# Kernel optimization log

Hardware: AMD Instinct MI355X
Metric: run time of the kernel (lower is better)

The kernel has to match this reference:

```python
import jax, jax.numpy as jnp
import numpy as np

B, L, DIN = 2048, 70, 15
HID, NF, K = 16, 4, 40          # hidden_units//2, n_features, kernel_size
C = DIN + 1 + NF                # 20 signature input channels (original + time + conv features)
Z0 = 64
SIG_CH = C + C * C + C ** 3     # 8420, depth-3 signature channels


def setup_inputs() -> dict:
    key = jax.random.key(0)
    ks = jax.random.split(key, 8)
    return {
        "observed_data": jax.random.normal(ks[0], (B, L, DIN), jnp.float32),
        "observed_tp": jnp.linspace(0.0, 1.0, L, dtype=jnp.float32),
        "conv1_w": jax.random.normal(ks[1], (HID, DIN, K), jnp.float32) / np.float32(np.sqrt(DIN * K)),
        "conv1_b": jnp.zeros((HID,), jnp.float32),
        "conv2_w": jax.random.normal(ks[2], (HID, HID), jnp.float32) / np.float32(np.sqrt(HID)),
        "conv2_b": jnp.zeros((HID,), jnp.float32),
        "conv3_w": jax.random.normal(ks[3], (NF, HID), jnp.float32) / np.float32(np.sqrt(HID)),
        "conv3_b": jnp.zeros((NF,), jnp.float32),
        "w_out": jax.random.normal(ks[4], (2 * Z0, SIG_CH), jnp.float32) * np.float32(np.sqrt(2.0 / (SIG_CH + 2 * Z0))),
        "b_out": jnp.zeros((2 * Z0,), jnp.float32),
    }


def _augment(x, w1, b1, w2, b2, w3, b3):
    # x: (B, L, DIN).  signatory.Augment: conv(K) -> relu -> conv1x1 -> relu -> conv1x1,
    # then concat [truncated original, time channel, conv features] along channels.
    xc = jnp.transpose(x, (0, 2, 1))                                   # (B, DIN, L)
    h = jax.lax.conv_general_dilated(xc, w1, (1,), 'VALID')            # (B, HID, Lp)
    h = h + b1[None, :, None]
    h = jnp.einsum('oc,bcl->bol', w2, jax.nn.relu(h)) + b2[None, :, None]
    h = jnp.einsum('oc,bcl->bol', w3, jax.nn.relu(h)) + b3[None, :, None]
    conv_out = jnp.transpose(h, (0, 2, 1))                             # (B, Lp, NF)
    Lp = conv_out.shape[1]
    orig = x[:, K - 1:, :]                                             # (B, Lp, DIN)
    t = jnp.linspace(0.0, 1.0, Lp, dtype=x.dtype)
    time = jnp.broadcast_to(t[None, :, None], (x.shape[0], Lp, 1))
    return jnp.concatenate([orig, time, conv_out], axis=2)             # (B, Lp, C)


def _signature_depth3(path):
    # Truncated (depth 3) path signature with basepoint=True, via Chen's identity:
    # S <- S \otimes exp(dx) over increments, zero basepoint prepended.
    incs = jnp.diff(path, axis=1, prepend=jnp.zeros_like(path[:, :1]))  # (B, Lp, C)
    incs = jnp.transpose(incs, (1, 0, 2))                               # (Lp, B, C)
    Bn, Cn = path.shape[0], path.shape[2]
    s1 = jnp.zeros((Bn, Cn), path.dtype)
    s2 = jnp.zeros((Bn, Cn, Cn), path.dtype)
    s3 = jnp.zeros((Bn, Cn, Cn, Cn), path.dtype)

    def step(carry, d):
        s1, s2, s3 = carry
        e2 = 0.5 * d[:, :, None] * d[:, None, :]                        # d\otimes d / 2
        e3 = (e2[:, :, :, None] * d[:, None, None, :]) / 3.0            # d^{\otimes 3} / 6
        n3 = (s3
              + s2[:, :, :, None] * d[:, None, None, :]
              + s1[:, :, None, None] * e2[:, None, :, :]
              + e3)
        n2 = s2 + s1[:, :, None] * d[:, None, :] + e2
        n1 = s1 + d
        return (n1, n2, n3), None

    (s1, s2, s3), _ = jax.lax.scan(step, (s1, s2, s3), incs)
    return jnp.concatenate([s1, s2.reshape(Bn, -1), s3.reshape(Bn, -1)], axis=1)


def reference(observed_data, observed_tp, conv1_w, conv1_b, conv2_w, conv2_b,
              conv3_w, conv3_b, w_out, b_out):
    # encode_obs_time=False -> observed_tp unused
    path = _augment(observed_data, conv1_w, conv1_b, conv2_w, conv2_b, conv3_w, conv3_b)
    sig = _signature_depth3(path)                                       # (B, SIG_CH)
    z = sig @ w_out.T + b_out                                           # (B, 2*Z0)
    mean_z0 = z[:, :Z0][None]                                           # (1, B, Z0)
    std_z0 = jax.nn.softplus(z[:, Z0:][None])                           # (1, B, Z0)
    return mean_z0, std_z0
```

## Files before the change

kernel.cpp:

```cpp
#include <hip/hip_runtime.h>
#include <math.h>

#define B_TOT 2048
#define D_INC 15
#define KW    40
#define CCH   20
#define LP    31
#define SIGCH 8420
#define SIGP  8448
#define NOUT  128
#define KSPLIT 11
#define KLEN  768

typedef _Float16 f16;
typedef _Float16 f16x8 __attribute__((ext_vector_type(8)));
typedef _Float16 f16x4 __attribute__((ext_vector_type(4)));
typedef _Float16 f16x2 __attribute__((ext_vector_type(2)));
typedef float    f32x4 __attribute__((ext_vector_type(4)));

__global__ __launch_bounds__(256) void k_prep(const float* __restrict__ w1,
                                              const float* __restrict__ w_out,
                                              f16* __restrict__ wA,
                                              f16* __restrict__ wh)
{
    if (blockIdx.x == 0) {
        const int ln = threadIdx.x & 63;
        const int wv = threadIdx.x >> 6;
        const int h  = ln & 15;
        const int q4 = ln >> 4;
        for (int gi = 0; gi < 5; ++gi) {
            int g = wv * 5 + gi;
            f16x8 v;
#pragma unroll
            for (int j = 0; j < 8; ++j) {
                int kq = q4 * 8 + j;
                int kk = 2 * g + (kq >> 4);
                int c  = kq & 15;
                v[j] = (c < D_INC) ? (f16)w1[h * 600 + c * 40 + kk] : (f16)0.f;
            }
            *(f16x8*)(wA + g * 512 + ln * 8) = v;
        }
        return;
    }
    int t0 = (blockIdx.x - 1) * 256 + threadIdx.x;
    for (int chunk = t0; chunk < 128 * 1056; chunk += 8192) {
        int o  = chunk / 1056;
        int cw = chunk - o * 1056;
        int c0 = cw * 8;
        f16x8 v;
        if (c0 + 8 <= SIGCH) {
            const float* src = w_out + (size_t)o * SIGCH + c0;
            float4 a = *(const float4*)src;
            float4 b = *(const float4*)(src + 4);
            v = (f16x8){(f16)a.x,(f16)a.y,(f16)a.z,(f16)a.w,
                        (f16)b.x,(f16)b.y,(f16)b.z,(f16)b.w};
        } else {
#pragma unroll
            for (int e = 0; e < 8; ++e) {
                int c = c0 + e;
                v[e] = (c < SIGCH) ? (f16)w_out[(size_t)o * SIGCH + c] : (f16)0.f;
            }
        }
        *(f16x8*)(wh + (size_t)o * SIGP + c0) = v;
    }
}

__global__ __launch_bounds__(256, 3) void k_augsig(
    const float* __restrict__ x,  const f16* __restrict__ wA, const float* __restrict__ b1,
    const float* __restrict__ w2, const float* __restrict__ b2,
    const float* __restrict__ w3, const float* __restrict__ b3,
    f16* __restrict__ sig)
{
    __shared__ float pool[12388];
    float* xs    = pool;
    f16*   xp16  = (f16*)(pool + 4272);
    float* h1s   = (float*)xp16;
    float* pprev = pool + 9408;
    float* wsmall= pool + 12032;
    float* w2s = wsmall;        float* b2s = wsmall + 256;
    float* w3s = wsmall + 272;  float* b3s = wsmall + 336;
    float* b1s = wsmall + 340;

    const int tid  = threadIdx.x;
    const int b0   = blockIdx.x * 4;
    const int lane = tid & 63;
    const int w    = tid >> 6;
    const int n16  = lane & 15;
    const int q4   = lane >> 4;

    for (int i = tid; i < 4 * 1050; i += 256) {
        int bl = i / 1050; int t = i - bl * 1050;
        xs[bl * 1068 + t] = x[(size_t)b0 * 1050 + i];
    }
    if (tid < 256) w2s[tid] = w2[tid];
    if (tid < 16)  b2s[tid] = b2[tid];
    if (tid < 64)  w3s[tid] = w3[tid];
    if (tid < 4)   b3s[tid] = b3[tid];
    if (tid < 16)  b1s[tid] = b1[tid];

    f16x8 wa[20];
#pragma unroll
    for (int g = 0; g < 20; ++g) wa[g] = *(const f16x8*)(wA + g * 512 + lane * 8);
    __syncthreads();

    for (int r = tid; r < 280; r += 256) {
        int bl = r / 70; int pos = r - bl * 70;
        const float* src = xs + bl * 1068 + pos * 15;
        f16* dst = xp16 + bl * 1152 + pos * 16;
#pragma unroll
        for (int c = 0; c < 15; ++c) dst[c] = (f16)src[c];
        dst[15] = (f16)0.f;
    }
    __syncthreads();

    f32x4 cacc[2];
#pragma unroll
    for (int tile = 0; tile < 2; ++tile) {
        const int pos0 = tile * 15;
        f32x4 acc = {0.f, 0.f, 0.f, 0.f};
#pragma unroll
        for (int g = 0; g < 20; ++g) {
            const f16x8 bf = *(const f16x8*)&xp16[w * 1152 +
                (pos0 + n16 + 2 * g + (q4 >> 1)) * 16 + (q4 & 1) * 8];
            acc = __builtin_amdgcn_mfma_f32_16x16x32_f16(wa[g], bf, acc, 0, 0, 0);
        }
        cacc[tile] = acc;
    }
    __syncthreads();

#pragma unroll
    for (int tile = 0; tile < 2; ++tile) {
        int pos = tile * 15 + n16;
#pragma unroll
        for (int r = 0; r < 4; ++r) {
            int h = q4 * 4 + r;
            h1s[(w * 31 + pos) * 17 + h] = fmaxf(cacc[tile][r] + b1s[h], 0.f);
        }
    }
    __syncthreads();

    if (tid < 124) {
        const int bl2 = tid / 31;
        const int pos = tid - bl2 * 31;
        float hr[16];
#pragma unroll
        for (int c2 = 0; c2 < 16; ++c2) hr[c2] = h1s[tid * 17 + c2];
        float h2[16];
#pragma unroll
        for (int o = 0; o < 16; ++o) {
            float s = b2s[o];
#pragma unroll
            for (int c2 = 0; c2 < 16; ++c2) s += w2s[o * 16 + c2] * hr[c2];
            h2[o] = fmaxf(s, 0.f);
        }
        float h3[4];
#pragma unroll
        for (int f = 0; f < 4; ++f) {
            float s = b3s[f];
#pragma unroll
            for (int c2 = 0; c2 < 16; ++c2) s += w3s[f * 16 + c2] * h2[c2];
            h3[f] = s;
        }
        float* pr = pprev + bl2 * 656 + 20 + pos * 20;
#pragma unroll
        for (int d = 0; d < D_INC; ++d) pr[d] = xs[bl2 * 1068 + (pos + 39) * 15 + d];
        pr[15] = (float)pos * (1.0f / 30.0f);
#pragma unroll
        for (int f = 0; f < 4; ++f) pr[16 + f] = h3[f];
    } else {
        int z = tid - 124;
        if (z < 80) pprev[(z / 20) * 656 + (z % 20)] = 0.f;
    }
    __syncthreads();

    float* pp   = pprev + w * 656;
    f16*   scr  = (f16*)pool + w * 4704;
    f16*   dtr  = scr;
    f16*   atr  = scr + 800;
    f16*   etr  = scr + 1600;
    f16*   Vb   = scr + 2400;

    for (int e = lane; e < 620; e += 64) {
        int c = e / 31, t = e - c * 31;
        float p0 = pp[t * 20 + c];
        float d  = pp[(t + 1) * 20 + c] - p0;
        dtr[c * 40 + t] = (f16)d;
        atr[c * 40 + t] = (f16)(p0 + 0.5f * d);
        etr[c * 40 + t] = (f16)(0.5f * p0 + d * (1.0f / 6.0f));
    }
    if (lane < 20) {
        dtr[lane * 40 + 31] = (f16)0.f;
        atr[lane * 40 + 31] = (f16)0.f;
        etr[lane * 40 + 31] = (f16)0.f;
    }
    __syncthreads();

    if (lane < 20) {
        f16* vr = Vb + lane * 72;
        float s = 0.f;
        for (int t = 30; t >= 0; --t) {
            float dv = (float)dtr[lane * 40 + t];
            vr[t]      = (f16)s;
            vr[32 + t] = (f16)dv;
            s += dv;
        }
        vr[31] = (f16)0.f;
        vr[63] = (f16)0.f;
    } else if (lane == 20) {
        f16* vr = Vb + 20 * 72;
        for (int k = 0; k < 64; ++k) vr[k] = (k < 31) ? (f16)1.f : (f16)0.f;
    }
    for (int e = lane; e < 11 * 32; e += 64) {
        int row = 21 + (e >> 5);
        int kk  = (e & 31) * 2;
        *(f16x2*)(Vb + row * 72 + kk) = (f16x2){(f16)0.f, (f16)0.f};
    }
    __syncthreads();

    f16x8 bf[2][2];
#pragma unroll
    for (int kc = 0; kc < 2; ++kc)
#pragma unroll
        for (int nt = 0; nt < 2; ++nt)
            bf[kc][nt] = *(const f16x8*)(Vb + (nt * 16 + n16) * 72 + kc * 32 + q4 * 8);

    const int b = b0 + w;
    f16* sg = sig + (size_t)b * SIGP;

    for (int mt = 0; mt < 25; ++mt) {
        const int p = mt * 16 + n16;
        const int i = p / 20, j = p - i * 20;
        f16x8 av = *(const f16x8*)(atr + i * 40 + q4 * 8);
        f16x8 ev = *(const f16x8*)(etr + i * 40 + q4 * 8);
        f16x8 dv = *(const f16x8*)(dtr + j * 40 + q4 * 8);
        f16x8 uf = av * dv;
        f16x8 ef = ev * dv;

        f32x4 a0 = {0.f,0.f,0.f,0.f}, a1 = {0.f,0.f,0.f,0.f};
        a0 = __builtin_amdgcn_mfma_f32_16x16x32_f16(bf[0][0], uf, a0, 0, 0, 0);
        a0 = __builtin_amdgcn_mfma_f32_16x16x32_f16(bf[1][0], ef, a0, 0, 0, 0);
        a1 = __builtin_amdgcn_mfma_f32_16x16x32_f16(bf[0][1], uf, a1, 0, 0, 0);
        a1 = __builtin_amdgcn_mfma_f32_16x16x32_f16(bf[1][1], ef, a1, 0, 0, 0);

        f16x4 s0 = {(f16)a0[0], (f16)a0[1], (f16)a0[2], (f16)a0[3]};
        *(f16x4*)(sg + 420 + p * 20 + q4 * 4) = s0;
        if (q4 == 0) {
            f16x4 s1v = {(f16)a1[0], (f16)a1[1], (f16)a1[2], (f16)a1[3]};
            *(f16x4*)(sg + 420 + p * 20 + 16) = s1v;
        } else if (q4 == 1) {
            sg[20 + p] = (f16)a1[0];
        }
    }

    if (lane < 20) sg[lane] = (f16)pp[620 + lane];
    if (lane < 28) sg[SIGCH + lane] = (f16)0.f;
}

__global__ __launch_bounds__(256, 4) void k_gemm(const f16* __restrict__ sigh,
                                                 const f16* __restrict__ wh,
                                                 float* __restrict__ z_part)
{
    const int tid = threadIdx.x;
    const int l   = tid & 63;
    const int wv  = tid >> 6;
    const int mt  = blockIdx.x / KSPLIT;
    const int s   = blockIdx.x - mt * KSPLIT;
    const int m0  = mt * 32;
    const int kb  = s * KLEN;
    const int kg   = l >> 4;
    const int mrow = l & 15;

    const f16* a0p = sigh + (size_t)(m0 + mrow) * SIGP + kb + kg * 8;
    const f16* a1p = a0p + (size_t)16 * SIGP;
    const f16* b0p = wh   + (size_t)(wv * 32 + mrow) * SIGP + kb + kg * 8;
    const f16* b1p = b0p + (size_t)16 * SIGP;

    const f32x4 z4 = {0.f, 0.f, 0.f, 0.f};
    f32x4 acc[2][2];
    acc[0][0] = z4; acc[0][1] = z4; acc[1][0] = z4; acc[1][1] = z4;

#pragma unroll 2
    for (int ks = 0; ks < 24; ++ks) {
        const int ko = ks * 32;
        f16x8 aF0 = *(const f16x8*)(a0p + ko);
        f16x8 aF1 = *(const f16x8*)(a1p + ko);
        f16x8 bF0 = *(const f16x8*)(b0p + ko);
        f16x8 bF1 = *(const f16x8*)(b1p + ko);
        acc[0][0] = __builtin_amdgcn_mfma_f32_16x16x32_f16(aF0, bF0, acc[0][0], 0, 0, 0);
        acc[0][1] = __builtin_amdgcn_mfma_f32_16x16x32_f16(aF0, bF1, acc[0][1], 0, 0, 0);
        acc[1][0] = __builtin_amdgcn_mfma_f32_16x16x32_f16(aF1, bF0, acc[1][0], 0, 0, 0);
        acc[1][1] = __builtin_amdgcn_mfma_f32_16x16x32_f16(aF1, bF1, acc[1][1], 0, 0, 0);
    }

#pragma unroll
    for (int m2 = 0; m2 < 2; ++m2) {
#pragma unroll
        for (int n2 = 0; n2 < 2; ++n2) {
            int n = wv * 32 + n2 * 16 + (l & 15);
#pragma unroll
            for (int r = 0; r < 4; ++r) {
                int m = m0 + m2 * 16 + (l >> 4) * 4 + r;
                z_part[((size_t)s * B_TOT + m) * NOUT + n] = acc[m2][n2][r];
            }
        }
    }
}

__global__ __launch_bounds__(256) void k_final(const float* __restrict__ z_part,
                                               const float* __restrict__ b_out,
                                               float* __restrict__ out)
{
    int idx = blockIdx.x * 256 + threadIdx.x;
    int b  = idx >> 5;
    int o4 = (idx & 31) << 2;
    float4 z = *(const float4*)(b_out + o4);
#pragma unroll
    for (int s = 0; s < KSPLIT; ++s) {
        const float4 p = *(const float4*)(z_part + ((size_t)s * B_TOT + b) * NOUT + o4);
        z.x += p.x; z.y += p.y; z.z += p.z; z.w += p.w;
    }
    if (o4 < 64) {
        *(float4*)(out + (size_t)b * 64 + o4) = z;
    } else {
        float4 sp;
        sp.x = fmaxf(z.x, 0.f) + log1pf(expf(-fabsf(z.x)));
        sp.y = fmaxf(z.y, 0.f) + log1pf(expf(-fabsf(z.y)));
        sp.z = fmaxf(z.z, 0.f) + log1pf(expf(-fabsf(z.z)));
        sp.w = fmaxf(z.w, 0.f) + log1pf(expf(-fabsf(z.w)));
        *(float4*)(out + 131072 + (size_t)b * 64 + (o4 - 64)) = sp;
    }
}

extern "C" void kernel_launch(void* const* d_in, const int* in_sizes, int n_in,
                              void* d_out, int out_size, void* d_ws, size_t ws_size,
                              hipStream_t stream)
{
    const float* x     = (const float*)d_in[0];
    const float* w1    = (const float*)d_in[2];
    const float* b1    = (const float*)d_in[3];
    const float* w2    = (const float*)d_in[4];
    const float* b2    = (const float*)d_in[5];
    const float* w3    = (const float*)d_in[6];
    const float* b3    = (const float*)d_in[7];
    const float* w_out = (const float*)d_in[8];
    const float* b_out = (const float*)d_in[9];
    float* out = (float*)d_out;

    float* ws    = (float*)d_ws;
    f16*   sigh  = (f16*)ws;
    f16*   wh    = (f16*)(ws + 8650752);
    f16*   wA    = (f16*)(ws + 9191424);
    float* zpart = ws + 9196544;

    hipLaunchKernelGGL(k_prep,   dim3(33),   dim3(256), 0, stream, w1, w_out, wA, wh);
    hipLaunchKernelGGL(k_augsig, dim3(512),  dim3(256), 0, stream,
                       x, wA, b1, w2, b2, w3, b3, sigh);
    hipLaunchKernelGGL(k_gemm,   dim3(704),  dim3(256), 0, stream, sigh, wh, zpart);
    hipLaunchKernelGGL(k_final,  dim3(256),  dim3(256), 0, stream, zpart, b_out, out);
}
```

Baseline: 144.8 us.

## Overlap w_out fp16 conversion with signature kernel and prefetch GEMM operands

```diff
diff --git a/kernel.cpp b/kernel.cpp
--- a/kernel.cpp
+++ b/kernel.cpp
@@ -19,49 +19,23 @@
 typedef float    f32x4 __attribute__((ext_vector_type(4)));
 
 __global__ __launch_bounds__(256) void k_prep(const float* __restrict__ w1,
-                                              const float* __restrict__ w_out,
-                                              f16* __restrict__ wA,
-                                              f16* __restrict__ wh)
-{
-    if (blockIdx.x == 0) {
-        const int ln = threadIdx.x & 63;
-        const int wv = threadIdx.x >> 6;
-        const int h  = ln & 15;
-        const int q4 = ln >> 4;
-        for (int gi = 0; gi < 5; ++gi) {
-            int g = wv * 5 + gi;
-            f16x8 v;
-#pragma unroll
-            for (int j = 0; j < 8; ++j) {
-                int kq = q4 * 8 + j;
-                int kk = 2 * g + (kq >> 4);
-                int c  = kq & 15;
-                v[j] = (c < D_INC) ? (f16)w1[h * 600 + c * 40 + kk] : (f16)0.f;
-            }
-            *(f16x8*)(wA + g * 512 + ln * 8) = v;
-        }
-        return;
-    }
-    int t0 = (blockIdx.x - 1) * 256 + threadIdx.x;
-    for (int chunk = t0; chunk < 128 * 1056; chunk += 8192) {
-        int o  = chunk / 1056;
-        int cw = chunk - o * 1056;
-        int c0 = cw * 8;
+                                              f16* __restrict__ wA)
+{
+    const int ln = threadIdx.x & 63;
+    const int wv = threadIdx.x >> 6;
+    const int h  = ln & 15;
+    const int q4 = ln >> 4;
+    for (int gi = 0; gi < 5; ++gi) {
+        int g = wv * 5 + gi;
         f16x8 v;
-        if (c0 + 8 <= SIGCH) {
-            const float* src = w_out + (size_t)o * SIGCH + c0;
-            float4 a = *(const float4*)src;
-            float4 b = *(const float4*)(src + 4);
-            v = (f16x8){(f16)a.x,(f16)a.y,(f16)a.z,(f16)a.w,
-                        (f16)b.x,(f16)b.y,(f16)b.z,(f16)b.w};
-        } else {
-#pragma unroll
-            for (int e = 0; e < 8; ++e) {
-                int c = c0 + e;
-                v[e] = (c < SIGCH) ? (f16)w_out[(size_t)o * SIGCH + c] : (f16)0.f;
-            }
-        }
-        *(f16x8*)(wh + (size_t)o * SIGP + c0) = v;
+#pragma unroll
+        for (int j = 0; j < 8; ++j) {
+            int kq = q4 * 8 + j;
+            int kk = 2 * g + (kq >> 4);
+            int c  = kq & 15;
+            v[j] = (c < D_INC) ? (f16)w1[h * 600 + c * 40 + kk] : (f16)0.f;
+        }
+        *(f16x8*)(wA + g * 512 + ln * 8) = v;
     }
 }
 
@@ -69,8 +43,33 @@
     const float* __restrict__ x,  const f16* __restrict__ wA, const float* __restrict__ b1,
     const float* __restrict__ w2, const float* __restrict__ b2,
     const float* __restrict__ w3, const float* __restrict__ b3,
-    f16* __restrict__ sig)
-{
+    const float* __restrict__ w_out, f16* __restrict__ wh, f16* __restrict__ sig)
+{
+    if (blockIdx.x >= 512) {
+        int t0 = (blockIdx.x - 512) * 256 + threadIdx.x;
+        for (int chunk = t0; chunk < 128 * 1056; chunk += 8192) {
+            int o  = chunk / 1056;
+            int cw = chunk - o * 1056;
+            int c0 = cw * 8;
+            f16x8 v;
+            if (c0 + 8 <= SIGCH) {
+                const float* src = w_out + (size_t)o * SIGCH + c0;
+                float4 a = *(const float4*)src;
+                float4 b = *(const float4*)(src + 4);
+                v = (f16x8){(f16)a.x,(f16)a.y,(f16)a.z,(f16)a.w,
+                            (f16)b.x,(f16)b.y,(f16)b.z,(f16)b.w};
+            } else {
+#pragma unroll
+                for (int e = 0; e < 8; ++e) {
+                    int c = c0 + e;
+                    v[e] = (c < SIGCH) ? (f16)w_out[(size_t)o * SIGCH + c] : (f16)0.f;
+                }
+            }
+            *(f16x8*)(wh + (size_t)o * SIGP + c0) = v;
+        }
+        return;
+    }
+
     __shared__ float pool[12388];
     float* xs    = pool;
     f16*   xp16  = (f16*)(pool + 4272);
@@ -256,9 +255,9 @@
     if (lane < 28) sg[SIGCH + lane] = (f16)0.f;
 }
 
-__global__ __launch_bounds__(256, 4) void k_gemm(const f16* __restrict__ sigh,
-                                                 const f16* __restrict__ wh,
-                                                 float* __restrict__ z_part)
+__global__ __launch_bounds__(256) void k_gemm(const f16* __restrict__ sigh,
+                                              const f16* __restrict__ wh,
+                                              float* __restrict__ z_part)
 {
     const int tid = threadIdx.x;
     const int l   = tid & 63;
@@ -276,31 +275,57 @@
     const f16* b1p = b0p + (size_t)16 * SIGP;
 
     const f32x4 z4 = {0.f, 0.f, 0.f, 0.f};
-    f32x4 acc[2][2];
-    acc[0][0] = z4; acc[0][1] = z4; acc[1][0] = z4; acc[1][1] = z4;
-
-#pragma unroll 2
-    for (int ks = 0; ks < 24; ++ks) {
-        const int ko = ks * 32;
-        f16x8 aF0 = *(const f16x8*)(a0p + ko);
-        f16x8 aF1 = *(const f16x8*)(a1p + ko);
-        f16x8 bF0 = *(const f16x8*)(b0p + ko);
-        f16x8 bF1 = *(const f16x8*)(b1p + ko);
-        acc[0][0] = __builtin_amdgcn_mfma_f32_16x16x32_f16(aF0, bF0, acc[0][0], 0, 0, 0);
-        acc[0][1] = __builtin_amdgcn_mfma_f32_16x16x32_f16(aF0, bF1, acc[0][1], 0, 0, 0);
-        acc[1][0] = __builtin_amdgcn_mfma_f32_16x16x32_f16(aF1, bF0, acc[1][0], 0, 0, 0);
-        acc[1][1] = __builtin_amdgcn_mfma_f32_16x16x32_f16(aF1, bF1, acc[1][1], 0, 0, 0);
+    f32x4 acc00 = z4, acc01 = z4, acc10 = z4, acc11 = z4;
+
+    f16x8 xa0 = *(const f16x8*)(a0p);
+    f16x8 xa1 = *(const f16x8*)(a1p);
+    f16x8 xb0 = *(const f16x8*)(b0p);
+    f16x8 xb1 = *(const f16x8*)(b1p);
+    f16x8 ya0 = *(const f16x8*)(a0p + 32);
+    f16x8 ya1 = *(const f16x8*)(a1p + 32);
+    f16x8 yb0 = *(const f16x8*)(b0p + 32);
+    f16x8 yb1 = *(const f16x8*)(b1p + 32);
+
+#pragma unroll
+    for (int it = 0; it < 12; ++it) {
+        f16x8 ua0 = xa0, ua1 = xa1, ub0 = xb0, ub1 = xb1;
+        if (it < 11) {
+            const int ko = (2 * it + 2) * 32;
+            xa0 = *(const f16x8*)(a0p + ko);
+            xa1 = *(const f16x8*)(a1p + ko);
+            xb0 = *(const f16x8*)(b0p + ko);
+            xb1 = *(const f16x8*)(b1p + ko);
+        }
+        acc00 = __builtin_amdgcn_mfma_f32_16x16x32_f16(ua0, ub0, acc00, 0, 0, 0);
+        acc01 = __builtin_amdgcn_mfma_f32_16x16x32_f16(ua0, ub1, acc01, 0, 0, 0);
+        acc10 = __builtin_amdgcn_mfma_f32_16x16x32_f16(ua1, ub0, acc10, 0, 0, 0);
+        acc11 = __builtin_amdgcn_mfma_f32_16x16x32_f16(ua1, ub1, acc11, 0, 0, 0);
+
+        f16x8 va0 = ya0, va1 = ya1, vb0 = yb0, vb1 = yb1;
+        if (it < 11) {
+            const int ko = (2 * it + 3) * 32;
+            ya0 = *(const f16x8*)(a0p + ko);
+            ya1 = *(const f16x8*)(a1p + ko);
+            yb0 = *(const f16x8*)(b0p + ko);
+            yb1 = *(const f16x8*)(b1p + ko);
+        }
+        acc00 = __builtin_amdgcn_mfma_f32_16x16x32_f16(va0, vb0, acc00, 0, 0, 0);
+        acc01 = __builtin_amdgcn_mfma_f32_16x16x32_f16(va0, vb1, acc01, 0, 0, 0);
+        acc10 = __builtin_amdgcn_mfma_f32_16x16x32_f16(va1, vb0, acc10, 0, 0, 0);
+        acc11 = __builtin_amdgcn_mfma_f32_16x16x32_f16(va1, vb1, acc11, 0, 0, 0);
     }
 
 #pragma unroll
     for (int m2 = 0; m2 < 2; ++m2) {
 #pragma unroll
         for (int n2 = 0; n2 < 2; ++n2) {
+            const f32x4 a = (m2 == 0) ? (n2 == 0 ? acc00 : acc01)
+                                      : (n2 == 0 ? acc10 : acc11);
             int n = wv * 32 + n2 * 16 + (l & 15);
 #pragma unroll
             for (int r = 0; r < 4; ++r) {
                 int m = m0 + m2 * 16 + (l >> 4) * 4 + r;
-                z_part[((size_t)s * B_TOT + m) * NOUT + n] = acc[m2][n2][r];
+                z_part[((size_t)s * B_TOT + m) * NOUT + n] = a[r];
             }
         }
     }
@@ -352,9 +377,9 @@
     f16*   wA    = (f16*)(ws + 9191424);
     float* zpart = ws + 9196544;
 
-    hipLaunchKernelGGL(k_prep,   dim3(33),   dim3(256), 0, stream, w1, w_out, wA, wh);
-    hipLaunchKernelGGL(k_augsig, dim3(512),  dim3(256), 0, stream,
-                       x, wA, b1, w2, b2, w3, b3, sigh);
+    hipLaunchKernelGGL(k_prep,   dim3(1),    dim3(256), 0, stream, w1, wA);
+    hipLaunchKernelGGL(k_augsig, dim3(544),  dim3(256), 0, stream,
+                       x, wA, b1, w2, b2, w3, b3, w_out, wh, sigh);
     hipLaunchKernelGGL(k_gemm,   dim3(704),  dim3(256), 0, stream, sigh, wh, zpart);
     hipLaunchKernelGGL(k_final,  dim3(256),  dim3(256), 0, stream, zpart, b_out, out);
 }
```

New measurement: 139.5 us. -3.7%, faster.
